# Kernel optimization log

Measured on AMD Instinct MI355X. Metric: run time of the kernel, lower is better.

Reference implementation:

```python
import jax, jax.numpy as jnp
import numpy as np

DIM = 256          # channels
HEADS = 8
KS = 3             # kernel_size
DIL = (1, 2, 3, 4) # dilation rates
ND = len(DIL)
HEAD_DIM = DIM // HEADS
SCALE = HEAD_DIM ** -0.5
DPG = DIM // ND    # channels per dilation group
EPS = 1e-5


def setup_inputs() -> dict:
    key = jax.random.key(0)
    ks = jax.random.split(key, 4)
    B, H, W = 8, 64, 64
    vi = jax.random.normal(ks[0], (B, DIM, H, W), jnp.float32)
    ir = jax.random.normal(ks[1], (B, DIM, H, W), jnp.float32)
    w_qkv = jax.random.normal(ks[2], (3 * DIM, DIM), jnp.float32) * 0.02  # 1x1 conv, no bias (qkv_bias=False)
    proj_w = jax.random.normal(ks[3], (DIM, DIM), jnp.float32) * 0.02     # nn.Linear weight
    proj_b = jnp.zeros((DIM,), jnp.float32)
    ln_g = jnp.ones((DIM,), jnp.float32)
    ln_b = jnp.zeros((DIM,), jnp.float32)
    return dict(vi=vi, ir=ir, w_qkv=w_qkv, proj_w=proj_w, proj_b=proj_b, ln_g=ln_g, ln_b=ln_b)


def _unfold(t, dil):
    # t: [B, d, H, W] -> [B, d, KS*KS, H, W], same layout as nn.Unfold(KS, dil, pad=dil*(KS-1)//2)
    B, d, H, W = t.shape
    pad = dil * (KS - 1) // 2
    tp = jnp.pad(t, ((0, 0), (0, 0), (pad, pad), (pad, pad)))
    patches = [tp[:, :, i * dil:i * dil + H, j * dil:j * dil + W]
               for i in range(KS) for j in range(KS)]
    return jnp.stack(patches, axis=2)


def _dilate_attention(q, k, v, dil):
    # q,k,v: [B, d, H, W] with d = DPG; returns [B, H, W, d]
    B, d, H, W = q.shape
    h = d // HEAD_DIM
    N = H * W
    kk = KS * KS
    qf = q.reshape(B, h, HEAD_DIM, N)                      # b h d n
    kf = _unfold(k, dil).reshape(B, h, HEAD_DIM, kk, N)    # b h d k n
    vf = _unfold(v, dil).reshape(B, h, HEAD_DIM, kk, N)
    attn = jax.nn.softmax(jnp.einsum('bhdn,bhdkn->bhnk', qf, kf) * SCALE, axis=-1)
    out = jnp.einsum('bhnk,bhdkn->bhnd', attn, vf)         # b h n d
    return out.transpose(0, 2, 1, 3).reshape(B, H, W, d)   # channel = head*HEAD_DIM + c


def _dilate_block(x, w_qkv, proj_w, proj_b, ln_g, ln_b):
    # x: [B, C, H, W]; DilateBlock: permute -> LN -> MultiDilatelocalAttention -> residual -> permute back
    B, C, H, W = x.shape
    xn = x.transpose(0, 2, 3, 1)                           # B H W C
    mu = jnp.mean(xn, -1, keepdims=True)
    var = jnp.var(xn, -1, keepdims=True)
    xn = (xn - mu) * jax.lax.rsqrt(var + EPS) * ln_g + ln_b
    xc = xn.transpose(0, 3, 1, 2)                          # B C H W
    # 1x1 conv qkv -> [B, 3, ND, DPG, H, W]
    qkv = jnp.einsum('oc,bchw->bohw', w_qkv, xc).reshape(B, 3, ND, DPG, H, W)
    outs = [_dilate_attention(qkv[:, 0, i], qkv[:, 1, i], qkv[:, 2, i], DIL[i])
            for i in range(ND)]                            # each [B, H, W, DPG]
    y = jnp.stack(outs, axis=3).reshape(B, H, W, C)        # channel = dil_idx*DPG + c
    y = y @ proj_w.T + proj_b                              # nn.Linear
    return x + y.transpose(0, 3, 1, 2)                     # residual, back to B C H W


def reference(vi, ir, w_qkv, proj_w, proj_b, ln_g, ln_b):
    sub = vi - ir
    div = _dilate_block(sub, w_qkv, proj_w, proj_b, ln_g, ln_b)
    o = jnp.matmul(vi, div)   # batched [H,W]@[H,W] over (B, C)
    return (o, o)
```

## Files before the change

kernel.cpp:

```cpp
#include <hip/hip_runtime.h>
#include <math.h>

#define B_ 8
#define C_ 256
#define N_ 4096
#define NPOS 32768
#define SCALE_ 0.1767766952966369f
#define EPS_ 1e-5f

typedef __attribute__((ext_vector_type(8))) short bf16x8;
typedef __attribute__((ext_vector_type(8))) unsigned short u16x8;
typedef __attribute__((ext_vector_type(4))) float f32x4;

__device__ __forceinline__ unsigned short f2bf(float f) {
  union { float f; unsigned u; } v; v.f = f;
  unsigned r = v.u + 0x7fff + ((v.u >> 16) & 1);
  return (unsigned short)(r >> 16);
}
__device__ __forceinline__ float bf2f(unsigned short u) {
  union { unsigned u; float f; } v; v.u = ((unsigned)u) << 16; return v.f;
}
__device__ __forceinline__ float blo(unsigned u) {
  union { unsigned u; float f; } v; v.u = u << 16; return v.f;
}
__device__ __forceinline__ float bhi(unsigned u) {
  union { unsigned u; float f; } v; v.u = u & 0xffff0000u; return v.f;
}

#define GLD_LDS16(g, l) \
  __builtin_amdgcn_global_load_lds((const __attribute__((address_space(1))) unsigned int*)(g), \
                                   (__attribute__((address_space(3))) unsigned int*)(l), 16, 0, 0)

__global__ __launch_bounds__(256) void k_pre(
    const float* __restrict__ vi, const float* __restrict__ ir,
    const float* __restrict__ wq, const float* __restrict__ pw,
    const float* __restrict__ ln_g, const float* __restrict__ ln_b,
    unsigned short* __restrict__ wdst,
    unsigned short* __restrict__ subB, unsigned short* __restrict__ viB,
    unsigned short* __restrict__ xn)
{
  __shared__ float tile[C_ * 33];
  __shared__ float redS[8][32], redS2[8][32];
  __shared__ float meanS[32], rstdS[32];
  int t = threadIdx.x;
  if (blockIdx.x < 256) {
    int i4 = blockIdx.x * 256 + t;
    float4 v = (i4 < 49152) ? ((const float4*)wq)[i4] : ((const float4*)pw)[i4 - 49152];
    ushort4 o;
    o.x = f2bf(v.x); o.y = f2bf(v.y); o.z = f2bf(v.z); o.w = f2bf(v.w);
    ((ushort4*)wdst)[i4] = o;
    return;
  }
  int blk = blockIdx.x - 256;
  int b = blk >> 7;
  int y = (blk >> 1) & 63;
  int half = blk & 1;
  size_t base = (size_t)b * C_ * N_ + (size_t)y * 64 + half * 32;
  #pragma unroll
  for (int it = 0; it < 8; ++it) {
    int c = it * 32 + (t >> 3);
    int xq = (t & 7) * 4;
    size_t g = base + (size_t)c * N_ + xq;
    float4 v4 = *(const float4*)&vi[g];
    float4 i4 = *(const float4*)&ir[g];
    float4 s4;
    s4.x = v4.x - i4.x; s4.y = v4.y - i4.y; s4.z = v4.z - i4.z; s4.w = v4.w - i4.w;
    ushort4 sb, vb;
    sb.x = f2bf(s4.x); sb.y = f2bf(s4.y); sb.z = f2bf(s4.z); sb.w = f2bf(s4.w);
    vb.x = f2bf(v4.x); vb.y = f2bf(v4.y); vb.z = f2bf(v4.z); vb.w = f2bf(v4.w);
    *(ushort4*)&subB[g] = sb;
    *(ushort4*)&viB[g] = vb;
    tile[c * 33 + xq + 0] = s4.x;
    tile[c * 33 + xq + 1] = s4.y;
    tile[c * 33 + xq + 2] = s4.z;
    tile[c * 33 + xq + 3] = s4.w;
  }
  __syncthreads();
  {
    int p = t & 31, grp = t >> 5;
    float s = 0.f, s2 = 0.f;
    #pragma unroll
    for (int cc = 0; cc < 32; ++cc) {
      float v = tile[(grp * 32 + cc) * 33 + p];
      s += v; s2 += v * v;
    }
    redS[grp][p] = s; redS2[grp][p] = s2;
  }
  __syncthreads();
  if (t < 32) {
    float s = 0.f, s2 = 0.f;
    #pragma unroll
    for (int g2 = 0; g2 < 8; ++g2) { s += redS[g2][t]; s2 += redS2[g2][t]; }
    float mu = s * (1.f / 256.f);
    float var = s2 * (1.f / 256.f) - mu * mu;
    meanS[t] = mu;
    rstdS[t] = rsqrtf(var + EPS_);
  }
  __syncthreads();
  int c = t;
  float gg = ln_g[c], bb = ln_b[c];
  size_t xbase = ((size_t)b * N_ + (size_t)y * 64 + half * 32) * C_;
  for (int p = 0; p < 32; ++p) {
    float v = (tile[c * 33 + p] - meanS[p]) * rstdS[p] * gg + bb;
    xn[xbase + (size_t)p * C_ + c] = f2bf(v);
  }
}

template<int EPI, int NT>
__global__ __launch_bounds__(256) void k_gemm_mfma(
    const unsigned short* __restrict__ A,
    const unsigned short* __restrict__ Bw,
    unsigned short* __restrict__ Cout,
    const float* __restrict__ bias,
    const unsigned short* __restrict__ subB,
    int ldc)
{
  __shared__ __align__(16) unsigned short As[128 * 32];
  __shared__ __align__(16) unsigned short Bs[128 * 32];
  __shared__ __align__(16) unsigned short Cs[64 * 136];
  int flat = blockIdx.x;
  int xcd = flat & 7;
  int l = flat >> 3;
  int ml = l / NT;
  int nn = l - ml * NT;
  int m0 = (xcd * 32 + ml) * 128;
  int n0 = nn * 128;
  int tid = threadIdx.x;
  int wv = tid >> 6;
  int lane = tid & 63;
  int mw = (wv >> 1) * 64, nw = (wv & 1) * 64;
  int r = lane & 15, q = lane >> 4;

  int seg0 = wv * 2;
  int srow0 = seg0 * 16 + (lane >> 2);
  int scol = (lane & 3) * 8;
  const unsigned short* ga0 = A  + (size_t)(m0 + srow0) * 256 + scol;
  const unsigned short* ga1 = ga0 + 16 * 256;
  const unsigned short* gb0 = Bw + (size_t)(n0 + srow0) * 256 + scol;
  const unsigned short* gb1 = gb0 + 16 * 256;
  unsigned short* la0 = &As[seg0 * 512];
  unsigned short* la1 = la0 + 512;
  unsigned short* lb0 = &Bs[seg0 * 512];
  unsigned short* lb1 = lb0 + 512;

  f32x4 acc[4][4];
  #pragma unroll
  for (int i = 0; i < 4; ++i)
    #pragma unroll
    for (int j = 0; j < 4; ++j)
      acc[i][j] = (f32x4){0.f, 0.f, 0.f, 0.f};

  for (int k0 = 0; k0 < 256; k0 += 32) {
    GLD_LDS16(ga0 + k0, la0);
    GLD_LDS16(ga1 + k0, la1);
    GLD_LDS16(gb0 + k0, lb0);
    GLD_LDS16(gb1 + k0, lb1);
    __syncthreads();
    bf16x8 af[4], bfr[4];
    #pragma unroll
    for (int mt = 0; mt < 4; ++mt)
      af[mt] = *(const bf16x8*)&As[(mw + mt * 16 + r) * 32 + q * 8];
    #pragma unroll
    for (int nt = 0; nt < 4; ++nt)
      bfr[nt] = *(const bf16x8*)&Bs[(nw + nt * 16 + r) * 32 + q * 8];
    #pragma unroll
    for (int mt = 0; mt < 4; ++mt)
      #pragma unroll
      for (int nt = 0; nt < 4; ++nt)
        acc[mt][nt] = __builtin_amdgcn_mfma_f32_16x16x32_bf16(af[mt], bfr[nt], acc[mt][nt], 0, 0, 0);
    __syncthreads();
  }

  int b = m0 >> 12;
  int nn0 = m0 & 4095;
  #pragma unroll
  for (int pass = 0; pass < 2; ++pass) {
    __syncthreads();
    if (EPI == 0) {
      if ((wv >> 1) == pass) {
        #pragma unroll
        for (int mt = 0; mt < 4; ++mt) {
          int lr = mt * 16 + q * 4;
          #pragma unroll
          for (int nt = 0; nt < 4; ++nt) {
            int col = nw + nt * 16 + r;
            #pragma unroll
            for (int rr = 0; rr < 4; ++rr)
              Cs[(lr + rr) * 136 + col] = f2bf(acc[mt][nt][rr]);
          }
        }
      }
    } else {
      if ((wv & 1) == pass) {
        #pragma unroll
        for (int nt = 0; nt < 4; ++nt) {
          int lr = nt * 16 + r;
          #pragma unroll
          for (int mt = 0; mt < 4; ++mt) {
            int pc = mw + mt * 16 + q * 4;
            #pragma unroll
            for (int rr = 0; rr < 4; ++rr)
              Cs[lr * 136 + pc + rr] = f2bf(acc[mt][nt][rr]);
          }
        }
      }
    }
    __syncthreads();
    if (EPI == 0) {
      #pragma unroll
      for (int cc = 0; cc < 4; ++cc) {
        int ch = cc * 256 + tid;
        int row = ch >> 4, cg = ch & 15;
        u16x8 cv = *(const u16x8*)&Cs[row * 136 + cg * 8];
        int m = m0 + pass * 64 + row;
        *(u16x8*)&Cout[(size_t)m * ldc + n0 + cg * 8] = cv;
      }
    } else {
      #pragma unroll
      for (int cc = 0; cc < 4; ++cc) {
        int ch = cc * 256 + tid;
        int row = ch >> 4, cg = ch & 15;
        u16x8 cv = *(const u16x8*)&Cs[row * 136 + cg * 8];
        int c = n0 + pass * 64 + row;
        size_t idx = ((size_t)(b * 256 + c)) * 4096 + nn0 + cg * 8;
        u16x8 sv = *(const u16x8*)&subB[idx];
        float bb = bias[c];
        u16x8 ov;
        #pragma unroll
        for (int e = 0; e < 8; ++e)
          ov[e] = f2bf(bf2f((unsigned short)cv[e]) + bb + bf2f((unsigned short)sv[e]));
        *(u16x8*)&Cout[idx] = ov;
      }
    }
  }
}

__global__ __launch_bounds__(256) void k_attn(
    const unsigned short* __restrict__ qkv,
    unsigned short* __restrict__ y)
{
  int t = threadIdx.x;
  int sub = t >> 2;
  int lane4 = t & 3;
  int item = blockIdx.x * 64 + sub;
  int ih = item & 7;
  int p = item >> 3;
  int i = ih >> 1, h = ih & 1;
  int dil = i + 1;
  int b = p >> 12;
  int n = p & 4095;
  int py = n >> 6, px = n & 63;
  int off = i * 64 + h * 32 + lane4 * 8;
  const unsigned short* base = qkv + off;

  uint4 qw = *(const uint4*)(base + (size_t)p * 768);
  float q0 = blo(qw.x), q1 = bhi(qw.x), q2 = blo(qw.y), q3 = bhi(qw.y),
        q4 = blo(qw.z), q5 = bhi(qw.z), q6 = blo(qw.w), q7 = bhi(qw.w);

  int pj[9];
  #pragma unroll
  for (int j = 0; j < 9; ++j) {
    int ny = py + (j / 3 - 1) * dil;
    int nx = px + (j % 3 - 1) * dil;
    bool ok = ((unsigned)ny < 64u) && ((unsigned)nx < 64u);
    pj[j] = ok ? ((b << 12) + (ny << 6) + nx) : -1;
  }

  float sc[9];
  #pragma unroll
  for (int j = 0; j < 9; ++j) {
    float s = 0.f;
    if (pj[j] >= 0) {
      uint4 kw = *(const uint4*)(base + 256 + (size_t)pj[j] * 768);
      s  = q0 * blo(kw.x) + q1 * bhi(kw.x);
      s += q2 * blo(kw.y) + q3 * bhi(kw.y);
      s += q4 * blo(kw.z) + q5 * bhi(kw.z);
      s += q6 * blo(kw.w) + q7 * bhi(kw.w);
    }
    s += __shfl_xor(s, 1, 4);
    s += __shfl_xor(s, 2, 4);
    sc[j] = s * SCALE_;
  }

  float mx = sc[0];
  #pragma unroll
  for (int j = 1; j < 9; ++j) mx = fmaxf(mx, sc[j]);
  float e[9], ssum = 0.f;
  #pragma unroll
  for (int j = 0; j < 9; ++j) { e[j] = __expf(sc[j] - mx); ssum += e[j]; }
  float inv = 1.f / ssum;

  float o0 = 0.f, o1 = 0.f, o2 = 0.f, o3 = 0.f, o4 = 0.f, o5 = 0.f, o6 = 0.f, o7 = 0.f;
  #pragma unroll
  for (int j = 0; j < 9; ++j) {
    if (pj[j] >= 0) {
      float w = e[j] * inv;
      uint4 vw = *(const uint4*)(base + 512 + (size_t)pj[j] * 768);
      o0 += w * blo(vw.x); o1 += w * bhi(vw.x);
      o2 += w * blo(vw.y); o3 += w * bhi(vw.y);
      o4 += w * blo(vw.z); o5 += w * bhi(vw.z);
      o6 += w * blo(vw.w); o7 += w * bhi(vw.w);
    }
  }

  u16x8 ov;
  ov[0] = f2bf(o0); ov[1] = f2bf(o1); ov[2] = f2bf(o2); ov[3] = f2bf(o3);
  ov[4] = f2bf(o4); ov[5] = f2bf(o5); ov[6] = f2bf(o6); ov[7] = f2bf(o7);
  *(u16x8*)(y + (size_t)p * 256 + off) = ov;
}

__global__ __launch_bounds__(256) void k_bmm(
    const unsigned short* __restrict__ viB,
    const unsigned short* __restrict__ divmB,
    float* __restrict__ out)
{
  __shared__ __align__(16) unsigned short Vs[64 * 72];
  __shared__ __align__(16) unsigned short Ds[64 * 72];
  int bc = blockIdx.x;
  size_t base = (size_t)bc * 4096;
  int t = threadIdx.x;
  {
    int flat = t * 16;
    int row = flat >> 6, col = flat & 63;
    u16x8 v0 = *(const u16x8*)&viB[base + flat];
    u16x8 v1 = *(const u16x8*)&viB[base + flat + 8];
    *(u16x8*)&Vs[row * 72 + col] = v0;
    *(u16x8*)&Vs[row * 72 + col + 8] = v1;
    u16x8 d0 = *(const u16x8*)&divmB[base + flat];
    u16x8 d1 = *(const u16x8*)&divmB[base + flat + 8];
    #pragma unroll
    for (int e = 0; e < 8; ++e) {
      Ds[(col + e) * 72 + row] = (unsigned short)d0[e];
      Ds[(col + 8 + e) * 72 + row] = (unsigned short)d1[e];
    }
  }
  __syncthreads();
  int w = t >> 6, lane = t & 63;
  int r = lane & 15, q = lane >> 4;
  int wi = (w >> 1) * 32, wj = (w & 1) * 32;
  f32x4 acc[2][2];
  #pragma unroll
  for (int i = 0; i < 2; ++i)
    #pragma unroll
    for (int j = 0; j < 2; ++j)
      acc[i][j] = (f32x4){0.f, 0.f, 0.f, 0.f};
  #pragma unroll
  for (int ks = 0; ks < 2; ++ks) {
    bf16x8 a[2], bfr[2];
    #pragma unroll
    for (int ti = 0; ti < 2; ++ti)
      a[ti] = *(const bf16x8*)&Vs[(wi + ti * 16 + r) * 72 + ks * 32 + q * 8];
    #pragma unroll
    for (int tj = 0; tj < 2; ++tj)
      bfr[tj] = *(const bf16x8*)&Ds[(wj + tj * 16 + r) * 72 + ks * 32 + q * 8];
    #pragma unroll
    for (int ti = 0; ti < 2; ++ti)
      #pragma unroll
      for (int tj = 0; tj < 2; ++tj)
        acc[ti][tj] = __builtin_amdgcn_mfma_f32_16x16x32_bf16(a[ti], bfr[tj], acc[ti][tj], 0, 0, 0);
  }
  #pragma unroll
  for (int ti = 0; ti < 2; ++ti)
    #pragma unroll
    for (int tj = 0; tj < 2; ++tj)
      #pragma unroll
      for (int rr = 0; rr < 4; ++rr) {
        int row = wi + ti * 16 + q * 4 + rr;
        int col = wj + tj * 16 + r;
        float v = acc[ti][tj][rr];
        out[base + row * 64 + col] = v;
        out[8388608ull + base + row * 64 + col] = v;
      }
}

extern "C" void kernel_launch(void* const* d_in, const int* in_sizes, int n_in,
                              void* d_out, int out_size, void* d_ws, size_t ws_size,
                              hipStream_t stream) {
  const float* vi     = (const float*)d_in[0];
  const float* ir     = (const float*)d_in[1];
  const float* w_qkv  = (const float*)d_in[2];
  const float* proj_w = (const float*)d_in[3];
  const float* proj_b = (const float*)d_in[4];
  const float* ln_g   = (const float*)d_in[5];
  const float* ln_b   = (const float*)d_in[6];
  float* out = (float*)d_out;
  char* ws = (char*)d_ws;
  unsigned short* subB = (unsigned short*)(ws);
  unsigned short* qkvb = (unsigned short*)(ws + 16777216);
  unsigned short* divmB= (unsigned short*)(ws + 16777216);
  unsigned short* xnb  = (unsigned short*)(ws + 67108864);
  unsigned short* yb   = (unsigned short*)(ws + 83886080);
  unsigned short* viB  = (unsigned short*)(ws + 100663296);
  unsigned short* wqb  = (unsigned short*)(ws + 117440512);
  unsigned short* pwb  = wqb + 196608;

  k_pre<<<1280, 256, 0, stream>>>(vi, ir, w_qkv, proj_w, ln_g, ln_b, wqb, subB, viB, xnb);
  k_gemm_mfma<0, 6><<<1536, 256, 0, stream>>>(xnb, wqb, qkvb, nullptr, nullptr, 768);
  k_attn<<<4096, 256, 0, stream>>>(qkvb, yb);
  k_gemm_mfma<1, 2><<<512, 256, 0, stream>>>(yb, pwb, divmB, proj_b, subB, 0);
  k_bmm<<<2048, 256, 0, stream>>>(viB, divmB, out);
}
```

Before: 211.4 us.

## Restructure LayerNorm prep kernel with shuffle reductions and vectorized transposed output

The preprocessing kernel now has each block handle 16 pixels instead of 32, which doubles the block count. Per-pixel mean and variance are computed in registers with wave shuffles instead of a second pass over an fp32 LDS tile. The tile is stored as bf16 in pixel-major layout, so the normalized output can be written as 16-byte vectors instead of scalar 2-byte stores. The final batched-matmul output stores are also made nontemporal. A side effect is that normalization now reads the bf16-rounded difference, which adds a little precision loss.

```diff
diff --git a/kernel.cpp b/kernel.cpp
--- a/kernel.cpp
+++ b/kernel.cpp
@@ -39,70 +39,94 @@
     unsigned short* __restrict__ subB, unsigned short* __restrict__ viB,
     unsigned short* __restrict__ xn)
 {
-  __shared__ float tile[C_ * 33];
-  __shared__ float redS[8][32], redS2[8][32];
-  __shared__ float meanS[32], rstdS[32];
+  __shared__ unsigned short tile[16 * 264];
+  __shared__ float redS[4][16], redS2[4][16];
+  __shared__ float meanS[16], rstdS[16];
   int t = threadIdx.x;
-  if (blockIdx.x < 256) {
-    int i4 = blockIdx.x * 256 + t;
+  if (blockIdx.x >= 2048) {
+    int i4 = (blockIdx.x - 2048) * 256 + t;
     float4 v = (i4 < 49152) ? ((const float4*)wq)[i4] : ((const float4*)pw)[i4 - 49152];
     ushort4 o;
     o.x = f2bf(v.x); o.y = f2bf(v.y); o.z = f2bf(v.z); o.w = f2bf(v.w);
     ((ushort4*)wdst)[i4] = o;
     return;
   }
-  int blk = blockIdx.x - 256;
-  int b = blk >> 7;
-  int y = (blk >> 1) & 63;
-  int half = blk & 1;
-  size_t base = (size_t)b * C_ * N_ + (size_t)y * 64 + half * 32;
-  #pragma unroll
-  for (int it = 0; it < 8; ++it) {
-    int c = it * 32 + (t >> 3);
-    int xq = (t & 7) * 4;
-    size_t g = base + (size_t)c * N_ + xq;
+  int blk = blockIdx.x;
+  int b = blk >> 8;
+  int y = (blk >> 2) & 63;
+  int qtr = blk & 3;
+  int x0 = qtr * 16;
+  int k = t & 3;
+  int w = t >> 6;
+  float ps[4] = {0.f, 0.f, 0.f, 0.f}, ps2[4] = {0.f, 0.f, 0.f, 0.f};
+  #pragma unroll
+  for (int it = 0; it < 4; ++it) {
+    int c = it * 64 + (t >> 2);
+    size_t g = (((size_t)(b * 256 + c)) << 12) + y * 64 + x0 + k * 4;
     float4 v4 = *(const float4*)&vi[g];
     float4 i4 = *(const float4*)&ir[g];
-    float4 s4;
-    s4.x = v4.x - i4.x; s4.y = v4.y - i4.y; s4.z = v4.z - i4.z; s4.w = v4.w - i4.w;
+    float s0 = v4.x - i4.x, s1 = v4.y - i4.y, s2 = v4.z - i4.z, s3 = v4.w - i4.w;
     ushort4 sb, vb;
-    sb.x = f2bf(s4.x); sb.y = f2bf(s4.y); sb.z = f2bf(s4.z); sb.w = f2bf(s4.w);
+    sb.x = f2bf(s0); sb.y = f2bf(s1); sb.z = f2bf(s2); sb.w = f2bf(s3);
     vb.x = f2bf(v4.x); vb.y = f2bf(v4.y); vb.z = f2bf(v4.z); vb.w = f2bf(v4.w);
     *(ushort4*)&subB[g] = sb;
     *(ushort4*)&viB[g] = vb;
-    tile[c * 33 + xq + 0] = s4.x;
-    tile[c * 33 + xq + 1] = s4.y;
-    tile[c * 33 + xq + 2] = s4.z;
-    tile[c * 33 + xq + 3] = s4.w;
+    int xl = k * 4;
+    tile[(xl + 0) * 264 + c] = sb.x;
+    tile[(xl + 1) * 264 + c] = sb.y;
+    tile[(xl + 2) * 264 + c] = sb.z;
+    tile[(xl + 3) * 264 + c] = sb.w;
+    ps[0] += s0; ps2[0] += s0 * s0;
+    ps[1] += s1; ps2[1] += s1 * s1;
+    ps[2] += s2; ps2[2] += s2 * s2;
+    ps[3] += s3; ps2[3] += s3 * s3;
+  }
+  #pragma unroll
+  for (int j = 0; j < 4; ++j) {
+    #pragma unroll
+    for (int m = 4; m < 64; m <<= 1) {
+      ps[j]  += __shfl_xor(ps[j],  m);
+      ps2[j] += __shfl_xor(ps2[j], m);
+    }
+  }
+  if ((t & 63) < 4) {
+    #pragma unroll
+    for (int j = 0; j < 4; ++j) {
+      redS[w][k * 4 + j]  = ps[j];
+      redS2[w][k * 4 + j] = ps2[j];
+    }
   }
   __syncthreads();
-  {
-    int p = t & 31, grp = t >> 5;
-    float s = 0.f, s2 = 0.f;
-    #pragma unroll
-    for (int cc = 0; cc < 32; ++cc) {
-      float v = tile[(grp * 32 + cc) * 33 + p];
-      s += v; s2 += v * v;
-    }
-    redS[grp][p] = s; redS2[grp][p] = s2;
-  }
-  __syncthreads();
-  if (t < 32) {
-    float s = 0.f, s2 = 0.f;
-    #pragma unroll
-    for (int g2 = 0; g2 < 8; ++g2) { s += redS[g2][t]; s2 += redS2[g2][t]; }
+  if (t < 16) {
+    float s = redS[0][t] + redS[1][t] + redS[2][t] + redS[3][t];
+    float s2 = redS2[0][t] + redS2[1][t] + redS2[2][t] + redS2[3][t];
     float mu = s * (1.f / 256.f);
     float var = s2 * (1.f / 256.f) - mu * mu;
     meanS[t] = mu;
     rstdS[t] = rsqrtf(var + EPS_);
   }
   __syncthreads();
-  int c = t;
-  float gg = ln_g[c], bb = ln_b[c];
-  size_t xbase = ((size_t)b * N_ + (size_t)y * 64 + half * 32) * C_;
-  for (int p = 0; p < 32; ++p) {
-    float v = (tile[c * 33 + p] - meanS[p]) * rstdS[p] * gg + bb;
-    xn[xbase + (size_t)p * C_ + c] = f2bf(v);
+  #pragma unroll
+  for (int it2 = 0; it2 < 2; ++it2) {
+    int item = it2 * 256 + t;
+    int p = item >> 5, cg = item & 31;
+    int c0 = cg * 8;
+    u16x8 tv = *(const u16x8*)&tile[p * 264 + c0];
+    float4 gl = *(const float4*)&ln_g[c0];
+    float4 gh = *(const float4*)&ln_g[c0 + 4];
+    float4 bl = *(const float4*)&ln_b[c0];
+    float4 bh = *(const float4*)&ln_b[c0 + 4];
+    float mu = meanS[p], rs = rstdS[p];
+    u16x8 ov;
+    ov[0] = f2bf((bf2f((unsigned short)tv[0]) - mu) * rs * gl.x + bl.x);
+    ov[1] = f2bf((bf2f((unsigned short)tv[1]) - mu) * rs * gl.y + bl.y);
+    ov[2] = f2bf((bf2f((unsigned short)tv[2]) - mu) * rs * gl.z + bl.z);
+    ov[3] = f2bf((bf2f((unsigned short)tv[3]) - mu) * rs * gl.w + bl.w);
+    ov[4] = f2bf((bf2f((unsigned short)tv[4]) - mu) * rs * gh.x + bh.x);
+    ov[5] = f2bf((bf2f((unsigned short)tv[5]) - mu) * rs * gh.y + bh.y);
+    ov[6] = f2bf((bf2f((unsigned short)tv[6]) - mu) * rs * gh.z + bh.z);
+    ov[7] = f2bf((bf2f((unsigned short)tv[7]) - mu) * rs * gh.w + bh.w);
+    *(u16x8*)&xn[((size_t)(b * 4096 + y * 64 + x0 + p)) * 256 + c0] = ov;
   }
 }
 
@@ -368,8 +392,8 @@
         int row = wi + ti * 16 + q * 4 + rr;
         int col = wj + tj * 16 + r;
         float v = acc[ti][tj][rr];
-        out[base + row * 64 + col] = v;
-        out[8388608ull + base + row * 64 + col] = v;
+        __builtin_nontemporal_store(v, &out[base + row * 64 + col]);
+        __builtin_nontemporal_store(v, &out[8388608ull + base + row * 64 + col]);
       }
 }
 
@@ -394,7 +418,7 @@
   unsigned short* wqb  = (unsigned short*)(ws + 117440512);
   unsigned short* pwb  = wqb + 196608;
 
-  k_pre<<<1280, 256, 0, stream>>>(vi, ir, w_qkv, proj_w, ln_g, ln_b, wqb, subB, viB, xnb);
+  k_pre<<<2304, 256, 0, stream>>>(vi, ir, w_qkv, proj_w, ln_g, ln_b, wqb, subB, viB, xnb);
   k_gemm_mfma<0, 6><<<1536, 256, 0, stream>>>(xnb, wqb, qkvb, nullptr, nullptr, 768);
   k_attn<<<4096, 256, 0, stream>>>(qkvb, yb);
   k_gemm_mfma<1, 2><<<512, 256, 0, stream>>>(yb, pwb, divmB, proj_b, subB, 0);
```

Result: slower. 220.3 us (+4.2%).
